# Kernel optimization log

Hardware: AMD Instinct MI355X
Metric: run time of the kernel (lower is better)

Reference implementation:

```python
import jax, jax.numpy as jnp
import numpy as np

N_NODES = 50000
N_EDGES = 600000
N_GRAPHS = 256


def gcn_conv(x, W, b, src, dst, n):
    # PyG GCNConv: out = D^{-1/2} (A + I) D^{-1/2} X W + b
    h = x @ W  # [N, out]
    deg = jax.ops.segment_sum(jnp.ones((src.shape[0],), h.dtype), dst, num_segments=n) + 1.0  # self-loop
    dinv = jax.lax.rsqrt(deg)  # deg >= 1 so safe
    msgs = h[src] * (dinv[src] * dinv[dst])[:, None]  # [E, out]
    agg = jax.ops.segment_sum(msgs, dst, num_segments=n)
    agg = agg + h * (dinv * dinv)[:, None]  # self-loop contribution
    return agg + b


def setup_inputs() -> dict:
    key = jax.random.key(0)
    ks = jax.random.split(key, 8)
    x = jax.random.normal(ks[0], (N_NODES, 1), dtype=jnp.float32)
    edge_index = jax.random.randint(ks[1], (2, N_EDGES), 0, N_NODES, dtype=jnp.int64)
    batch = jnp.sort(jax.random.randint(ks[2], (N_NODES,), 0, N_GRAPHS, dtype=jnp.int64))

    def glorot(k, shape):
        lim = np.sqrt(6.0 / (shape[0] + shape[1]))
        return jax.random.uniform(k, shape, jnp.float32, -lim, lim)

    return {
        "x": x,
        "W1": glorot(ks[3], (1, 64)), "b1": jnp.zeros((64,), jnp.float32),
        "W2": glorot(ks[4], (64, 128)), "b2": jnp.zeros((128,), jnp.float32),
        "W3": glorot(ks[5], (128, 64)), "b3": jnp.zeros((64,), jnp.float32),
        "lin1_w": glorot(ks[6], (64, 32)), "lin1_b": jnp.zeros((32,), jnp.float32),
        "lin2_w": glorot(ks[7], (32, 1)), "lin2_b": jnp.zeros((1,), jnp.float32),
        "edge_index": edge_index,
        "batch": batch,
    }


def reference(x, W1, b1, W2, b2, W3, b3, lin1_w, lin1_b, lin2_w, lin2_b, edge_index, batch):
    src, dst = edge_index[0], edge_index[1]
    n = x.shape[0]
    h = jax.nn.relu(gcn_conv(x, W1, b1, src, dst, n))
    h = jax.nn.relu(gcn_conv(h, W2, b2, src, dst, n))
    h = jax.nn.relu(gcn_conv(h, W3, b3, src, dst, n))
    # global_mean_pool
    sums = jax.ops.segment_sum(h, batch, num_segments=N_GRAPHS)
    cnts = jax.ops.segment_sum(jnp.ones((n,), h.dtype), batch, num_segments=N_GRAPHS)
    pooled = sums / jnp.maximum(cnts, 1.0)[:, None]  # [G, 64]
    z = jax.nn.relu(pooled @ lin1_w + lin1_b)
    return z @ lin2_w + lin2_b  # [G, 1]
```

## Files before the change

### kernel.cpp

```cpp
#include <hip/hip_runtime.h>
#include <hip/hip_fp16.h>


#define N_FEAT 64
#define POOL_SUB 16
#define SLOT 64

__global__ void fill_kernel(const int* __restrict__ src, const int* __restrict__ dst,
                            int* __restrict__ deg, int* __restrict__ csr, int E) {
    int e4 = (blockIdx.x * blockDim.x + threadIdx.x) * 4;
    if (e4 + 3 < E) {
        int4 sv = *(const int4*)&src[e4];
        int4 dv = *(const int4*)&dst[e4];
        int p0 = atomicAdd(&deg[dv.x], 1);
        int p1 = atomicAdd(&deg[dv.y], 1);
        int p2 = atomicAdd(&deg[dv.z], 1);
        int p3 = atomicAdd(&deg[dv.w], 1);
        csr[dv.x * SLOT + p0] = sv.x;
        csr[dv.y * SLOT + p1] = sv.y;
        csr[dv.z * SLOT + p2] = sv.z;
        csr[dv.w * SLOT + p3] = sv.w;
    } else {
        for (int e = e4; e < E; ++e) {
            int d = dst[e];
            int pos = atomicAdd(&deg[d], 1);
            csr[d * SLOT + pos] = src[e];
        }
    }
}

__global__ void prep_kernel(const int* __restrict__ deg, const float* __restrict__ x,
                            float* __restrict__ dinv, float* __restrict__ xd, int N) {
    int i = blockIdx.x * blockDim.x + threadIdx.x;
    if (i < N) {
        float dv = rsqrtf((float)deg[i] + 1.0f);
        dinv[i] = dv;
        xd[i] = x[i] * dv;
    }
}

__global__ void sagg_gather(const int* __restrict__ deg, const int* __restrict__ csr,
                            const float* __restrict__ xd, const float* __restrict__ dinv,
                            float2* __restrict__ sd, int N) {
    int wid = (blockIdx.x * blockDim.x + threadIdx.x) >> 6;
    int lane = threadIdx.x & 63;
    int v = wid * 4 + (lane >> 4);
    int sub = lane & 15;
    if (v >= N) return;
    int dg = deg[v];
    int base = v * SLOT;
    float sum = 0.0f;
    for (int j = sub; j < dg; j += 16) sum += xd[csr[base + j]];
    #pragma unroll
    for (int off = 8; off; off >>= 1) sum += __shfl_xor(sum, off);
    if (sub == 0) {
        float dv = dinv[v];
        sd[v] = make_float2(dv * (sum + xd[v]), dv);
    }
}

__global__ void agg1_gather(const int* __restrict__ deg, const int* __restrict__ csr,
                            const float2* __restrict__ sd,
                            const float* __restrict__ W1, const float* __restrict__ b1,
                            float* __restrict__ agg, int N) {
    int wave = (blockIdx.x * blockDim.x + threadIdx.x) >> 6;
    int lane = threadIdx.x & 63;
    int v = wave * 2 + (lane >> 5);
    int sub = lane & 31;
    if (v >= N) return;
    float2 w  = *(const float2*)&W1[sub * 2];
    float2 bb = *(const float2*)&b1[sub * 2];
    int dg = deg[v];
    int base = v * SLOT;
    float ax = 0.0f, ay = 0.0f;
    int j = 0;
    for (; j + 3 < dg; j += 4) {
        int4 u = *(const int4*)&csr[base + j];
        float2 p0 = sd[u.x];
        float2 p1 = sd[u.y];
        float2 p2 = sd[u.z];
        float2 p3 = sd[u.w];
        ax += fmaxf(p0.x * w.x + bb.x, 0.0f) * p0.y + fmaxf(p1.x * w.x + bb.x, 0.0f) * p1.y;
        ax += fmaxf(p2.x * w.x + bb.x, 0.0f) * p2.y + fmaxf(p3.x * w.x + bb.x, 0.0f) * p3.y;
        ay += fmaxf(p0.x * w.y + bb.y, 0.0f) * p0.y + fmaxf(p1.x * w.y + bb.y, 0.0f) * p1.y;
        ay += fmaxf(p2.x * w.y + bb.y, 0.0f) * p2.y + fmaxf(p3.x * w.y + bb.y, 0.0f) * p3.y;
    }
    for (; j < dg; ++j) {
        float2 p = sd[csr[base + j]];
        ax += fmaxf(p.x * w.x + bb.x, 0.0f) * p.y;
        ay += fmaxf(p.x * w.y + bb.y, 0.0f) * p.y;
    }
    float2 pv = sd[v];
    float dv = pv.y;
    float2 o;
    o.x = dv * ax + fmaxf(pv.x * w.x + bb.x, 0.0f) * dv * dv;
    o.y = dv * ay + fmaxf(pv.x * w.y + bb.y, 0.0f) * dv * dv;
    *(float2*)&agg[(size_t)v * N_FEAT + sub * 2] = o;
}

#define H2S 132
#define BM 32
__global__ __launch_bounds__(256) void gemm12(const float* __restrict__ A,
                                              const float* __restrict__ W2,
                                              const float* __restrict__ bias2,
                                              const float* __restrict__ W3,
                                              const float* __restrict__ dinv,
                                              __half* __restrict__ md, int M) {
    __shared__ float Ws[128 * 64];
    __shared__ float Hs[BM * H2S];
    int tid = threadIdx.x;
    int row0 = blockIdx.x * BM;

    for (int idx = tid; idx < 64 * 128; idx += 256) Ws[idx] = W2[idx];
    {
        int r = tid >> 3;
        int kk = (tid & 7) * 8;
        int grow = row0 + r;
        float4 v0 = make_float4(0.f, 0.f, 0.f, 0.f), v1 = v0;
        if (grow < M) {
            v0 = *(const float4*)&A[(size_t)grow * 64 + kk];
            v1 = *(const float4*)&A[(size_t)grow * 64 + kk + 4];
        }
        *(float4*)&Hs[r * 64 + kk] = v0;
        *(float4*)&Hs[r * 64 + kk + 4] = v1;
    }
    __syncthreads();

    int c = (tid & 31) * 4;
    int rb = (tid >> 5) * 4;
    float acc1[4][4] = {};
    for (int k0 = 0; k0 < 64; k0 += 4) {
        float4 b0 = *(const float4*)&Ws[(k0 + 0) * 128 + c];
        float4 b1v = *(const float4*)&Ws[(k0 + 1) * 128 + c];
        float4 b2v = *(const float4*)&Ws[(k0 + 2) * 128 + c];
        float4 b3v = *(const float4*)&Ws[(k0 + 3) * 128 + c];
        #pragma unroll
        for (int i = 0; i < 4; ++i) {
            float4 a = *(const float4*)&Hs[(rb + i) * 64 + k0];
            acc1[i][0] += a.x * b0.x + a.y * b1v.x + a.z * b2v.x + a.w * b3v.x;
            acc1[i][1] += a.x * b0.y + a.y * b1v.y + a.z * b2v.y + a.w * b3v.y;
            acc1[i][2] += a.x * b0.z + a.y * b1v.z + a.z * b2v.z + a.w * b3v.z;
            acc1[i][3] += a.x * b0.w + a.y * b1v.w + a.z * b2v.w + a.w * b3v.w;
        }
    }
    float4 bv = *(const float4*)&bias2[c];
    __syncthreads();

    #pragma unroll
    for (int i = 0; i < 4; ++i) {
        float4 o;
        o.x = fmaxf(acc1[i][0] + bv.x, 0.f);
        o.y = fmaxf(acc1[i][1] + bv.y, 0.f);
        o.z = fmaxf(acc1[i][2] + bv.z, 0.f);
        o.w = fmaxf(acc1[i][3] + bv.w, 0.f);
        *(float4*)&Hs[(rb + i) * H2S + c] = o;
    }
    for (int idx = tid; idx < 128 * 64; idx += 256) Ws[idx] = W3[idx];
    __syncthreads();

    int c2 = (tid & 15) * 4;
    int r2 = (tid >> 4) * 2;
    float acc2[2][4] = {};
    for (int k0 = 0; k0 < 128; k0 += 4) {
        float4 w0 = *(const float4*)&Ws[(k0 + 0) * 64 + c2];
        float4 w1 = *(const float4*)&Ws[(k0 + 1) * 64 + c2];
        float4 w2 = *(const float4*)&Ws[(k0 + 2) * 64 + c2];
        float4 w3 = *(const float4*)&Ws[(k0 + 3) * 64 + c2];
        #pragma unroll
        for (int i = 0; i < 2; ++i) {
            float4 a = *(const float4*)&Hs[(r2 + i) * H2S + k0];
            acc2[i][0] += a.x * w0.x + a.y * w1.x + a.z * w2.x + a.w * w3.x;
            acc2[i][1] += a.x * w0.y + a.y * w1.y + a.z * w2.y + a.w * w3.y;
            acc2[i][2] += a.x * w0.z + a.y * w1.z + a.z * w2.z + a.w * w3.z;
            acc2[i][3] += a.x * w0.w + a.y * w1.w + a.z * w2.w + a.w * w3.w;
        }
    }
    #pragma unroll
    for (int i = 0; i < 2; ++i) {
        int grow = row0 + r2 + i;
        if (grow < M) {
            float dv = dinv[grow];
            __half2* p = (__half2*)&md[(size_t)grow * 64 + c2];
            p[0] = __floats2half2_rn(acc2[i][0] * dv, acc2[i][1] * dv);
            p[1] = __floats2half2_rn(acc2[i][2] * dv, acc2[i][3] * dv);
        }
    }
}

__global__ void agg3_gather(const int* __restrict__ deg, const int* __restrict__ csr,
                            const __half* __restrict__ md, const float* __restrict__ dinv,
                            float* __restrict__ agg, int N) {
    int wave = (blockIdx.x * blockDim.x + threadIdx.x) >> 6;
    int lane = threadIdx.x & 63;
    int v = wave * 4 + (lane >> 4);
    int sub = lane & 15;
    if (v >= N) return;
    const uint2* mdp = (const uint2*)md;
    int dg = deg[v];
    int base = v * SLOT;
    uint2 sv = mdp[(size_t)v * 16 + sub];
    float2 f0 = __half22float2(*(const __half2*)&sv.x);
    float2 f1 = __half22float2(*(const __half2*)&sv.y);
    float a0 = f0.x, a1 = f0.y, a2 = f1.x, a3 = f1.y;
    int j = 0;
    for (; j + 3 < dg; j += 4) {
        int4 u = *(const int4*)&csr[base + j];
        uint2 x0 = mdp[(size_t)u.x * 16 + sub];
        uint2 x1 = mdp[(size_t)u.y * 16 + sub];
        uint2 x2 = mdp[(size_t)u.z * 16 + sub];
        uint2 x3 = mdp[(size_t)u.w * 16 + sub];
        float2 p0 = __half22float2(*(const __half2*)&x0.x), q0 = __half22float2(*(const __half2*)&x0.y);
        float2 p1 = __half22float2(*(const __half2*)&x1.x), q1 = __half22float2(*(const __half2*)&x1.y);
        float2 p2 = __half22float2(*(const __half2*)&x2.x), q2 = __half22float2(*(const __half2*)&x2.y);
        float2 p3 = __half22float2(*(const __half2*)&x3.x), q3 = __half22float2(*(const __half2*)&x3.y);
        a0 += (p0.x + p1.x) + (p2.x + p3.x);
        a1 += (p0.y + p1.y) + (p2.y + p3.y);
        a2 += (q0.x + q1.x) + (q2.x + q3.x);
        a3 += (q0.y + q1.y) + (q2.y + q3.y);
    }
    for (; j < dg; ++j) {
        uint2 xv = mdp[(size_t)csr[base + j] * 16 + sub];
        float2 t0 = __half22float2(*(const __half2*)&xv.x);
        float2 t1 = __half22float2(*(const __half2*)&xv.y);
        a0 += t0.x; a1 += t0.y; a2 += t1.x; a3 += t1.y;
    }
    float dv = dinv[v];
    *(float4*)&agg[(size_t)v * N_FEAT + sub * 4] =
        make_float4(a0 * dv, a1 * dv, a2 * dv, a3 * dv);
}

__global__ void pool_kernel(const float* __restrict__ agg, const float* __restrict__ b3,
                            const int* __restrict__ batch, float* __restrict__ pooled,
                            float* __restrict__ counts, int N) {
    int wave = (blockIdx.x * blockDim.x + threadIdx.x) >> 6;
    int lane = threadIdx.x & 63;
    int start = wave * POOL_SUB;
    if (start >= N) return;
    int end = min(start + POOL_SUB, N);
    float bl = b3[lane];
    int cur = batch[start];
    float acc = 0.0f;
    float cnt = 0.0f;
    for (int i = start; i < end; ++i) {
        int g = batch[i];
        if (g != cur) {
            atomicAdd(&pooled[cur * N_FEAT + lane], acc);
            if (lane == 0) atomicAdd(&counts[cur], cnt);
            acc = 0.0f; cnt = 0.0f; cur = g;
        }
        acc += fmaxf(agg[(size_t)i * N_FEAT + lane] + bl, 0.0f);
        cnt += 1.0f;
    }
    atomicAdd(&pooled[cur * N_FEAT + lane], acc);
    if (lane == 0) atomicAdd(&counts[cur], cnt);
}

__global__ void mlp_kernel(const float* __restrict__ pooled, const float* __restrict__ counts,
                           const float* __restrict__ l1w, const float* __restrict__ l1b,
                           const float* __restrict__ l2w, const float* __restrict__ l2b,
                           float* __restrict__ out) {
    __shared__ float row[64];
    __shared__ float zs[32];
    int g = blockIdx.x;
    int l = threadIdx.x;
    float cnt = fmaxf(counts[g], 1.0f);
    row[l] = pooled[g * 64 + l] / cnt;
    __syncthreads();
    if (l < 32) {
        float z = l1b[l];
        #pragma unroll
        for (int k = 0; k < 64; ++k) z += row[k] * l1w[k * 32 + l];
        zs[l] = fmaxf(z, 0.0f);
    }
    __syncthreads();
    if (l == 0) {
        float o = l2b[0];
        #pragma unroll
        for (int j = 0; j < 32; ++j) o += zs[j] * l2w[j];
        out[g] = o;
    }
}

extern "C" void kernel_launch(void* const* d_in, const int* in_sizes, int n_in,
                              void* d_out, int out_size, void* d_ws, size_t ws_size,
                              hipStream_t stream) {
    const float* x   = (const float*)d_in[0];
    const float* W1  = (const float*)d_in[1];
    const float* b1  = (const float*)d_in[2];
    const float* W2  = (const float*)d_in[3];
    const float* b2  = (const float*)d_in[4];
    const float* W3  = (const float*)d_in[5];
    const float* b3  = (const float*)d_in[6];
    const float* l1w = (const float*)d_in[7];
    const float* l1b = (const float*)d_in[8];
    const float* l2w = (const float*)d_in[9];
    const float* l2b = (const float*)d_in[10];
    const int* ei    = (const int*)d_in[11];
    const int* batch = (const int*)d_in[12];

    int N = in_sizes[0];
    int E = in_sizes[11] / 2;
    int G = out_size;
    const int* src = ei;
    const int* dst = ei + E;

    char* wsb = (char*)d_ws;
    int*   deg      = (int*)wsb;                 wsb += (size_t)N * 4;
    float* pooled   = (float*)wsb;               wsb += (size_t)G * 64 * 4;
    float* counts   = (float*)wsb;               wsb += (size_t)G * 4;
    int*   csr      = (int*)wsb;                 wsb += (size_t)N * SLOT * 4;
    float* dinv     = (float*)wsb;               wsb += (size_t)N * 4;
    float* xd       = (float*)wsb;               wsb += (size_t)N * 4;
    float2* sd      = (float2*)wsb;              wsb += (size_t)N * 8;
    float* agg      = (float*)wsb;               wsb += (size_t)N * 64 * 4;
    __half* md      = (__half*)wsb;              wsb += (size_t)N * 64 * 2;

    hipMemsetAsync(deg, 0, ((size_t)N + (size_t)G * 64 + G) * 4, stream);

    int tb = 256;
    fill_kernel<<<(E / 4 + tb - 1) / tb, tb, 0, stream>>>(src, dst, deg, csr, E);
    prep_kernel<<<(N + tb - 1) / tb, tb, 0, stream>>>(deg, x, dinv, xd, N);
    sagg_gather<<<((N + 3) / 4 + 3) / 4, tb, 0, stream>>>(deg, csr, xd, dinv, sd, N);
    int a1_waves = (N + 1) / 2;
    agg1_gather<<<(a1_waves + 3) / 4, tb, 0, stream>>>(deg, csr, sd, W1, b1, agg, N);
    gemm12<<<(N + BM - 1) / BM, tb, 0, stream>>>(agg, W2, b2, W3, dinv, md, N);
    int a3_waves = (N + 3) / 4;
    agg3_gather<<<(a3_waves + 3) / 4, tb, 0, stream>>>(deg, csr, md, dinv, agg, N);
    int pool_waves = (N + POOL_SUB - 1) / POOL_SUB;
    pool_kernel<<<(pool_waves + 3) / 4, tb, 0, stream>>>(agg, b3, batch, pooled, counts, N);
    mlp_kernel<<<G, 64, 0, stream>>>(pooled, counts, l1w, l1b, l2w, l2b, (float*)d_out);
}
```

Before: 213.9 us.

## Use fp16 MFMA for fused two-layer GEMM with prepacked weights

Replaces the scalar FP32 LDS-tiled GEMM chain (agg@W2, relu, @W3) with MFMA 16x16x16 fp16 instructions. agg1 now writes its intermediate activations in fp16, halving that buffer's traffic, and prep_kernel packs W2/W3 into MFMA fragment order in fp16. This removes the weight staging in LDS and the FP32 FMA cost. It adds fp16 rounding of activations and weights, which may loosen accuracy.

```diff
diff --git a/kernel.cpp b/kernel.cpp
--- a/kernel.cpp
+++ b/kernel.cpp
@@ -5,6 +5,9 @@
 #define N_FEAT 64
 #define POOL_SUB 16
 #define SLOT 64
+
+typedef _Float16 f16x4 __attribute__((ext_vector_type(4)));
+typedef float f32x4 __attribute__((ext_vector_type(4)));
 
 __global__ void fill_kernel(const int* __restrict__ src, const int* __restrict__ dst,
                             int* __restrict__ deg, int* __restrict__ csr, int E) {
@@ -30,12 +33,32 @@
 }
 
 __global__ void prep_kernel(const int* __restrict__ deg, const float* __restrict__ x,
-                            float* __restrict__ dinv, float* __restrict__ xd, int N) {
+                            float* __restrict__ dinv, float* __restrict__ xd,
+                            const float* __restrict__ W2, const float* __restrict__ W3,
+                            __half* __restrict__ W2p, __half* __restrict__ W3p, int N) {
     int i = blockIdx.x * blockDim.x + threadIdx.x;
     if (i < N) {
         float dv = rsqrtf((float)deg[i] + 1.0f);
         dinv[i] = dv;
         xd[i] = x[i] * dv;
+    }
+    if (i < 16384) {
+        if (i < 8192) {
+            int ii = i & 3;
+            int lane = (i >> 2) & 63;
+            int blk = i >> 8;
+            int k = (blk & 3) * 16 + (lane >> 4) * 4 + ii;
+            int col = (blk >> 2) * 16 + (lane & 15);
+            W2p[i] = __float2half(W2[k * 128 + col]);
+        } else {
+            int t2 = i - 8192;
+            int ii = t2 & 3;
+            int lane = (t2 >> 2) & 63;
+            int blk = t2 >> 8;
+            int k = (blk & 7) * 16 + (lane >> 4) * 4 + ii;
+            int col = (blk >> 3) * 16 + (lane & 15);
+            W3p[t2] = __float2half(W3[k * 64 + col]);
+        }
     }
 }
 
@@ -62,7 +85,7 @@
 __global__ void agg1_gather(const int* __restrict__ deg, const int* __restrict__ csr,
                             const float2* __restrict__ sd,
                             const float* __restrict__ W1, const float* __restrict__ b1,
-                            float* __restrict__ agg, int N) {
+                            __half* __restrict__ agg16, int N) {
     int wave = (blockIdx.x * blockDim.x + threadIdx.x) >> 6;
     int lane = threadIdx.x & 63;
     int v = wave * 2 + (lane >> 5);
@@ -92,99 +115,79 @@
     }
     float2 pv = sd[v];
     float dv = pv.y;
-    float2 o;
-    o.x = dv * ax + fmaxf(pv.x * w.x + bb.x, 0.0f) * dv * dv;
-    o.y = dv * ay + fmaxf(pv.x * w.y + bb.y, 0.0f) * dv * dv;
-    *(float2*)&agg[(size_t)v * N_FEAT + sub * 2] = o;
-}
-
-#define H2S 132
-#define BM 32
-__global__ __launch_bounds__(256) void gemm12(const float* __restrict__ A,
-                                              const float* __restrict__ W2,
+    float ox = dv * ax + fmaxf(pv.x * w.x + bb.x, 0.0f) * dv * dv;
+    float oy = dv * ay + fmaxf(pv.x * w.y + bb.y, 0.0f) * dv * dv;
+    *(__half2*)&agg16[(size_t)v * N_FEAT + sub * 2] = __floats2half2_rn(ox, oy);
+}
+
+#define H2PAD 136
+__global__ __launch_bounds__(256) void gemm12(const __half* __restrict__ A16,
+                                              const __half* __restrict__ W2p,
                                               const float* __restrict__ bias2,
-                                              const float* __restrict__ W3,
+                                              const __half* __restrict__ W3p,
                                               const float* __restrict__ dinv,
                                               __half* __restrict__ md, int M) {
-    __shared__ float Ws[128 * 64];
-    __shared__ float Hs[BM * H2S];
+    __shared__ __half h2s[32 * H2PAD];
     int tid = threadIdx.x;
-    int row0 = blockIdx.x * BM;
-
-    for (int idx = tid; idx < 64 * 128; idx += 256) Ws[idx] = W2[idx];
-    {
-        int r = tid >> 3;
-        int kk = (tid & 7) * 8;
-        int grow = row0 + r;
-        float4 v0 = make_float4(0.f, 0.f, 0.f, 0.f), v1 = v0;
-        if (grow < M) {
-            v0 = *(const float4*)&A[(size_t)grow * 64 + kk];
-            v1 = *(const float4*)&A[(size_t)grow * 64 + kk + 4];
-        }
-        *(float4*)&Hs[r * 64 + kk] = v0;
-        *(float4*)&Hs[r * 64 + kk + 4] = v1;
+    int wave = tid >> 6, lane = tid & 63;
+    int g = lane >> 4, r = lane & 15;
+    int row0 = blockIdx.x * 32;
+
+    f16x4 af[2][4];
+    #pragma unroll
+    for (int rt = 0; rt < 2; ++rt) {
+        int row = row0 + rt * 16 + r;
+        if (row >= M) row = M - 1;
+        const __half* ap = A16 + (size_t)row * 64 + g * 4;
+        #pragma unroll
+        for (int kc = 0; kc < 4; ++kc)
+            af[rt][kc] = *(const f16x4*)(ap + kc * 16);
+    }
+
+    f32x4 acc[2][2] = {};
+    const f16x4* w2v = (const f16x4*)W2p;
+    #pragma unroll
+    for (int ctl = 0; ctl < 2; ++ctl) {
+        int ct = wave * 2 + ctl;
+        #pragma unroll
+        for (int kc = 0; kc < 4; ++kc) {
+            f16x4 bf = w2v[(ct * 4 + kc) * 64 + lane];
+            acc[0][ctl] = __builtin_amdgcn_mfma_f32_16x16x16f16(af[0][kc], bf, acc[0][ctl], 0, 0, 0);
+            acc[1][ctl] = __builtin_amdgcn_mfma_f32_16x16x16f16(af[1][kc], bf, acc[1][ctl], 0, 0, 0);
+        }
+    }
+    #pragma unroll
+    for (int ctl = 0; ctl < 2; ++ctl) {
+        int col = (wave * 2 + ctl) * 16 + r;
+        float bb = bias2[col];
+        #pragma unroll
+        for (int rt = 0; rt < 2; ++rt)
+            #pragma unroll
+            for (int i = 0; i < 4; ++i)
+                h2s[(rt * 16 + g * 4 + i) * H2PAD + col] =
+                    __float2half(fmaxf(acc[rt][ctl][i] + bb, 0.f));
     }
     __syncthreads();
 
-    int c = (tid & 31) * 4;
-    int rb = (tid >> 5) * 4;
-    float acc1[4][4] = {};
-    for (int k0 = 0; k0 < 64; k0 += 4) {
-        float4 b0 = *(const float4*)&Ws[(k0 + 0) * 128 + c];
-        float4 b1v = *(const float4*)&Ws[(k0 + 1) * 128 + c];
-        float4 b2v = *(const float4*)&Ws[(k0 + 2) * 128 + c];
-        float4 b3v = *(const float4*)&Ws[(k0 + 3) * 128 + c];
+    f32x4 acc2[2] = {};
+    const f16x4* w3v = (const f16x4*)W3p;
+    #pragma unroll
+    for (int kc = 0; kc < 8; ++kc) {
+        f16x4 bf = w3v[(wave * 8 + kc) * 64 + lane];
+        #pragma unroll
+        for (int rt = 0; rt < 2; ++rt) {
+            f16x4 a2 = *(const f16x4*)&h2s[(rt * 16 + r) * H2PAD + kc * 16 + g * 4];
+            acc2[rt] = __builtin_amdgcn_mfma_f32_16x16x16f16(a2, bf, acc2[rt], 0, 0, 0);
+        }
+    }
+    #pragma unroll
+    for (int rt = 0; rt < 2; ++rt)
         #pragma unroll
         for (int i = 0; i < 4; ++i) {
-            float4 a = *(const float4*)&Hs[(rb + i) * 64 + k0];
-            acc1[i][0] += a.x * b0.x + a.y * b1v.x + a.z * b2v.x + a.w * b3v.x;
-            acc1[i][1] += a.x * b0.y + a.y * b1v.y + a.z * b2v.y + a.w * b3v.y;
-            acc1[i][2] += a.x * b0.z + a.y * b1v.z + a.z * b2v.z + a.w * b3v.z;
-            acc1[i][3] += a.x * b0.w + a.y * b1v.w + a.z * b2v.w + a.w * b3v.w;
-        }
-    }
-    float4 bv = *(const float4*)&bias2[c];
-    __syncthreads();
-
-    #pragma unroll
-    for (int i = 0; i < 4; ++i) {
-        float4 o;
-        o.x = fmaxf(acc1[i][0] + bv.x, 0.f);
-        o.y = fmaxf(acc1[i][1] + bv.y, 0.f);
-        o.z = fmaxf(acc1[i][2] + bv.z, 0.f);
-        o.w = fmaxf(acc1[i][3] + bv.w, 0.f);
-        *(float4*)&Hs[(rb + i) * H2S + c] = o;
-    }
-    for (int idx = tid; idx < 128 * 64; idx += 256) Ws[idx] = W3[idx];
-    __syncthreads();
-
-    int c2 = (tid & 15) * 4;
-    int r2 = (tid >> 4) * 2;
-    float acc2[2][4] = {};
-    for (int k0 = 0; k0 < 128; k0 += 4) {
-        float4 w0 = *(const float4*)&Ws[(k0 + 0) * 64 + c2];
-        float4 w1 = *(const float4*)&Ws[(k0 + 1) * 64 + c2];
-        float4 w2 = *(const float4*)&Ws[(k0 + 2) * 64 + c2];
-        float4 w3 = *(const float4*)&Ws[(k0 + 3) * 64 + c2];
-        #pragma unroll
-        for (int i = 0; i < 2; ++i) {
-            float4 a = *(const float4*)&Hs[(r2 + i) * H2S + k0];
-            acc2[i][0] += a.x * w0.x + a.y * w1.x + a.z * w2.x + a.w * w3.x;
-            acc2[i][1] += a.x * w0.y + a.y * w1.y + a.z * w2.y + a.w * w3.y;
-            acc2[i][2] += a.x * w0.z + a.y * w1.z + a.z * w2.z + a.w * w3.z;
-            acc2[i][3] += a.x * w0.w + a.y * w1.w + a.z * w2.w + a.w * w3.w;
-        }
-    }
-    #pragma unroll
-    for (int i = 0; i < 2; ++i) {
-        int grow = row0 + r2 + i;
-        if (grow < M) {
-            float dv = dinv[grow];
-            __half2* p = (__half2*)&md[(size_t)grow * 64 + c2];
-            p[0] = __floats2half2_rn(acc2[i][0] * dv, acc2[i][1] * dv);
-            p[1] = __floats2half2_rn(acc2[i][2] * dv, acc2[i][3] * dv);
-        }
-    }
+            int row = row0 + rt * 16 + g * 4 + i;
+            if (row < M)
+                md[(size_t)row * 64 + wave * 16 + r] = __float2half(acc2[rt][i] * dinv[row]);
+        }
 }
 
 __global__ void agg3_gather(const int* __restrict__ deg, const int* __restrict__ csr,
@@ -314,16 +317,19 @@
     float2* sd      = (float2*)wsb;              wsb += (size_t)N * 8;
     float* agg      = (float*)wsb;               wsb += (size_t)N * 64 * 4;
     __half* md      = (__half*)wsb;              wsb += (size_t)N * 64 * 2;
+    __half* agg16   = (__half*)wsb;              wsb += ((size_t)N + 32) * 64 * 2;
+    __half* W2p     = (__half*)wsb;              wsb += 8192 * 2;
+    __half* W3p     = (__half*)wsb;              wsb += 8192 * 2;
 
     hipMemsetAsync(deg, 0, ((size_t)N + (size_t)G * 64 + G) * 4, stream);
 
     int tb = 256;
     fill_kernel<<<(E / 4 + tb - 1) / tb, tb, 0, stream>>>(src, dst, deg, csr, E);
-    prep_kernel<<<(N + tb - 1) / tb, tb, 0, stream>>>(deg, x, dinv, xd, N);
+    prep_kernel<<<(N + tb - 1) / tb, tb, 0, stream>>>(deg, x, dinv, xd, W2, W3, W2p, W3p, N);
     sagg_gather<<<((N + 3) / 4 + 3) / 4, tb, 0, stream>>>(deg, csr, xd, dinv, sd, N);
     int a1_waves = (N + 1) / 2;
-    agg1_gather<<<(a1_waves + 3) / 4, tb, 0, stream>>>(deg, csr, sd, W1, b1, agg, N);
-    gemm12<<<(N + BM - 1) / BM, tb, 0, stream>>>(agg, W2, b2, W3, dinv, md, N);
+    agg1_gather<<<(a1_waves + 3) / 4, tb, 0, stream>>>(deg, csr, sd, W1, b1, agg16, N);
+    gemm12<<<(N + 31) / 32, tb, 0, stream>>>(agg16, W2p, b2, W3p, dinv, md, N);
     int a3_waves = (N + 3) / 4;
     agg3_gather<<<(a3_waves + 3) / 4, tb, 0, stream>>>(deg, csr, md, dinv, agg, N);
     int pool_waves = (N + POOL_SUB - 1) / POOL_SUB;
```

After: 196.7 us. 8.0% less time.
